# Performance work log

Hardware: AMD Instinct MI355X
Metric: run time of the kernel (lower is better)

The kernel has to match this reference:

```python
import jax, jax.numpy as jnp
import numpy as np

N = 100000      # num POIs (nodes)
M = 20000       # num trajectories (hyperedges)
NNZ = 1000000   # incidence entries
D = 128         # emb_dim
NUM_LAYERS = 3
NEG_SLOPE = 0.2  # PyG HypergraphConv leaky_relu default


def setup_inputs() -> dict:
    key = jax.random.key(0)
    ks = jax.random.split(key, 8)
    pois_embs = jax.random.normal(ks[0], (N, D), jnp.float32)
    traj_embs = jax.random.normal(ks[1], (M, D), jnp.float32)
    hyperedge_weight = jax.random.uniform(ks[2], (M,), jnp.float32)
    node_idx = jax.random.randint(ks[3], (NNZ,), 0, N, jnp.int32)
    edge_idx = jax.random.randint(ks[4], (NNZ,), 0, M, jnp.int32)
    # learned params of the shared HypergraphConv layer (heads=1, concat)
    W_lin = jax.random.normal(ks[5], (D, D), jnp.float32) / np.sqrt(D).astype(np.float32)
    att = jax.random.normal(ks[6], (2 * D,), jnp.float32) * 0.1
    bias = jnp.zeros((D,), jnp.float32)
    return dict(pois_embs=pois_embs, traj_embs=traj_embs,
                hyperedge_weight=hyperedge_weight,
                node_idx=node_idx, edge_idx=edge_idx,
                W_lin=W_lin, att=att, bias=bias)


def _segment_softmax(scores, seg, num_seg):
    smax = jax.ops.segment_max(scores, seg, num_segments=num_seg)
    smax = jnp.where(jnp.isfinite(smax), smax, 0.0)  # guard empty segments
    ex = jnp.exp(scores - smax[seg])
    den = jax.ops.segment_sum(ex, seg, num_segments=num_seg)
    return ex / (den[seg] + 1e-16)


def _hconv(x, traj_embs, hyperedge_weight, node_idx, edge_idx, W_lin, att, bias):
    # x: [N, D] node feats; traj_embs: [M, D] hyperedge feats
    xt = x @ W_lin            # [N, D]  lin(x)
    et = traj_embs @ W_lin    # [M, D]  lin(hyperedge_attr)
    # attention logits per incidence pair (additive decomposition of cat*att)
    s_n = xt @ att[:D]        # [N]
    s_e = et @ att[D:]        # [M]
    alpha = jax.nn.leaky_relu(s_n[node_idx] + s_e[edge_idx], NEG_SLOPE)  # [NNZ]
    alpha = _segment_softmax(alpha, node_idx, N)  # softmax grouped by node
    # degree normalizations: D = sum_e H_ve * w_e, B = |e|
    Ddeg = jax.ops.segment_sum(hyperedge_weight[edge_idx], node_idx, num_segments=N)
    Dinv = jnp.where(Ddeg > 0, 1.0 / Ddeg, 0.0)
    Bdeg = jax.ops.segment_sum(jnp.ones((NNZ,), xt.dtype), edge_idx, num_segments=M)
    Binv = jnp.where(Bdeg > 0, 1.0 / Bdeg, 0.0)
    # node -> edge: B^{-1} H^T (alpha * x)
    msg1 = (alpha * Binv[edge_idx])[:, None] * xt[node_idx]        # [NNZ, D]
    edge_out = jax.ops.segment_sum(msg1, edge_idx, num_segments=M)  # [M, D]
    # edge -> node: D^{-1} H (alpha * edge_out)
    msg2 = (alpha * Dinv[node_idx])[:, None] * edge_out[edge_idx]   # [NNZ, D]
    out = jax.ops.segment_sum(msg2, node_idx, num_segments=N)       # [N, D]
    return out + bias


def reference(pois_embs, traj_embs, hyperedge_weight, node_idx, edge_idx, W_lin, att, bias):
    cur = pois_embs
    acc = pois_embs  # running sum of stacked layer outputs (incl. input)
    for _ in range(NUM_LAYERS):
        cur = _hconv(cur, traj_embs, hyperedge_weight, node_idx, edge_idx, W_lin, att, bias) + cur
        acc = acc + cur
    return acc / jnp.asarray(NUM_LAYERS + 1, acc.dtype)  # mean over stack
```

## Files before the change

kernel.cpp:

```cpp
#include <hip/hip_runtime.h>
#include <cstdint>
#include <cstddef>

#define DIM 128
#define NEG_SLOPE 0.2f

typedef __attribute__((ext_vector_type(8))) short short8v;
typedef __attribute__((ext_vector_type(4))) float float4v;

__device__ __forceinline__ float bf_lo(uint u) { return __uint_as_float(u << 16); }
__device__ __forceinline__ float bf_hi(uint u) { return __uint_as_float(u & 0xffff0000u); }
__device__ __forceinline__ uint f2bf(float f) {
  uint u = __float_as_uint(f);
  return (u + 0x7fffu + ((u >> 16) & 1u)) >> 16;
}
__device__ __forceinline__ uint pack_bf2(float lo, float hi) {
  return f2bf(lo) | (f2bf(hi) << 16);
}
__device__ __forceinline__ float lrelu(float x) {
  return x >= 0.0f ? x : NEG_SLOPE * x;
}

__global__ void wswz_kernel(const float* __restrict__ W, ushort* __restrict__ Wswz)
{
  int i = blockIdx.x * 256 + threadIdx.x;
  int j = i & 7, lane = (i >> 3) & 63, nt = (i >> 9) & 7, kt = i >> 12;
  int k = kt * 32 + (lane >> 4) * 8 + j;
  int col = nt * 16 + (lane & 15);
  Wswz[i] = (ushort)f2bf(W[k * 128 + col]);
}

__global__ void poisbf_kernel(const float* __restrict__ pois,
                              uint4* __restrict__ pois_bf, int N_, int NP)
{
  int i = blockIdx.x * 256 + threadIdx.x;
  if (i >= NP * 16) return;
  int row = i >> 4;
  uint4 o;
  if (row < N_) {
    const float* src = pois + (size_t)i * 8;
    float4 f0 = *(const float4*)src;
    float4 f1 = *(const float4*)(src + 4);
    o.x = pack_bf2(f0.x, f0.y); o.y = pack_bf2(f0.z, f0.w);
    o.z = pack_bf2(f1.x, f1.y); o.w = pack_bf2(f1.z, f1.w);
  } else { o.x = o.y = o.z = o.w = 0; }
  pois_bf[i] = o;
}

__global__ __launch_bounds__(256) void gemm_mfma_kernel(
    const ushort* __restrict__ Xb, const ushort* __restrict__ Wswz,
    const float* __restrict__ att, ushort* __restrict__ Yb,
    float* __restrict__ s_n, int rowsN)
{
  __shared__ ushort st[64 * 128];
  int tid = threadIdx.x;
  int w = tid >> 6, lane = tid & 63;
  int q = lane >> 4, c = lane & 15;
  int r0b = blockIdx.x * 64;
  int r0 = r0b + w * 16;
  float4v acc[8];
#pragma unroll
  for (int nt = 0; nt < 8; ++nt) acc[nt] = (float4v){0.f, 0.f, 0.f, 0.f};
  const ushort* arow = Xb + (size_t)(r0 + c) * DIM + q * 8;
#pragma unroll
  for (int kt = 0; kt < 4; ++kt) {
    short8v a = *(const short8v*)(arow + kt * 32);
#pragma unroll
    for (int nt = 0; nt < 8; ++nt) {
      short8v b = *(const short8v*)(Wswz + ((((kt << 3) + nt) << 9) + (lane << 3)));
      acc[nt] = __builtin_amdgcn_mfma_f32_16x16x32_bf16(a, b, acc[nt], 0, 0, 0);
    }
  }
  float av[8];
#pragma unroll
  for (int nt = 0; nt < 8; ++nt) av[nt] = att[nt * 16 + c];
  float p0 = 0, p1 = 0, p2 = 0, p3 = 0;
#pragma unroll
  for (int nt = 0; nt < 8; ++nt) {
    p0 = fmaf(acc[nt][0], av[nt], p0);
    p1 = fmaf(acc[nt][1], av[nt], p1);
    p2 = fmaf(acc[nt][2], av[nt], p2);
    p3 = fmaf(acc[nt][3], av[nt], p3);
  }
#pragma unroll
  for (int m = 8; m >= 1; m >>= 1) {
    p0 += __shfl_xor(p0, m, 64);
    p1 += __shfl_xor(p1, m, 64);
    p2 += __shfl_xor(p2, m, 64);
    p3 += __shfl_xor(p3, m, 64);
  }
  if (c == 0) {
    int rb = r0 + q * 4;
    if (rb + 0 < rowsN) s_n[rb + 0] = p0;
    if (rb + 1 < rowsN) s_n[rb + 1] = p1;
    if (rb + 2 < rowsN) s_n[rb + 2] = p2;
    if (rb + 3 < rowsN) s_n[rb + 3] = p3;
  }
  ushort* sw = st + w * 2048;
#pragma unroll
  for (int nt = 0; nt < 8; ++nt) {
    sw[(q * 4 + 0) * 128 + nt * 16 + c] = (ushort)f2bf(acc[nt][0]);
    sw[(q * 4 + 1) * 128 + nt * 16 + c] = (ushort)f2bf(acc[nt][1]);
    sw[(q * 4 + 2) * 128 + nt * 16 + c] = (ushort)f2bf(acc[nt][2]);
    sw[(q * 4 + 3) * 128 + nt * 16 + c] = (ushort)f2bf(acc[nt][3]);
  }
  __syncthreads();
#pragma unroll
  for (int it = 0; it < 4; ++it) {
    int idx = tid + it * 256;
    int row = idx >> 4, seg = idx & 15;
    *(uint4*)(Yb + (size_t)(r0b + row) * DIM + seg * 8) =
        *(const uint4*)&st[row * 128 + seg * 8];
  }
}

__global__ __launch_bounds__(256) void se_kernel(
    const float* __restrict__ traj, const float* __restrict__ W,
    const float* __restrict__ att, const float* __restrict__ hw,
    float* __restrict__ s_e, float2* __restrict__ se_hw, int M_)
{
  __shared__ float wv[128];
  int tid = threadIdx.x;
  if (tid < 128) {
    const float* wr = W + (size_t)tid * 128;
    float acc = 0.0f;
#pragma unroll 4
    for (int k = 0; k < 128; ++k) acc = fmaf(wr[k], att[DIM + k], acc);
    wv[tid] = acc;
  }
  __syncthreads();
  int e = blockIdx.x * 4 + (tid >> 6);
  int lane = tid & 63;
  if (e >= M_) return;
  const float* row = traj + (size_t)e * DIM;
  float v = row[lane] * wv[lane] + row[lane + 64] * wv[lane + 64];
#pragma unroll
  for (int d = 32; d > 0; d >>= 1) v += __shfl_down(v, d, 64);
  if (lane == 0) {
    s_e[e] = v;
    float2 g; g.x = v; g.y = hw[e];
    se_hw[e] = g;
  }
}

__global__ void hist_rank_kernel(const int* __restrict__ node_idx,
                                 const int* __restrict__ edge_idx,
                                 int* __restrict__ ncnt, int* __restrict__ ecnt,
                                 int* __restrict__ r_n, int* __restrict__ r_e,
                                 int nnz)
{
  int j = (blockIdx.x * blockDim.x + threadIdx.x) * 2;
  if (j >= nnz) return;
  if (j + 2 <= nnz) {
    int2 e = *(const int2*)&edge_idx[j];
    int2 n = *(const int2*)&node_idx[j];
    int a0 = atomicAdd(&ecnt[e.x], 1);
    int a1 = atomicAdd(&ecnt[e.y], 1);
    int b0 = atomicAdd(&ncnt[n.x], 1);
    int b1 = atomicAdd(&ncnt[n.y], 1);
    *(int2*)&r_e[j] = make_int2(a0, a1);
    *(int2*)&r_n[j] = make_int2(b0, b1);
  } else {
    r_e[j] = atomicAdd(&ecnt[edge_idx[j]], 1);
    r_n[j] = atomicAdd(&ncnt[node_idx[j]], 1);
  }
}

__global__ __launch_bounds__(1024) void scan_block_kernel(
    const int* __restrict__ cnt, int* __restrict__ off,
    int* __restrict__ partials, int nbins)
{
  __shared__ int ws[16];
  int tid = threadIdx.x, lane = tid & 63, wid = tid >> 6;
  int base = blockIdx.x * 4096 + tid * 4;
  int x0 = base + 0 < nbins ? cnt[base + 0] : 0;
  int x1 = base + 1 < nbins ? cnt[base + 1] : 0;
  int x2 = base + 2 < nbins ? cnt[base + 2] : 0;
  int x3 = base + 3 < nbins ? cnt[base + 3] : 0;
  int t = x0 + x1 + x2 + x3;
  int v = t;
#pragma unroll
  for (int d = 1; d < 64; d <<= 1) {
    int y = __shfl_up(v, d, 64);
    if (lane >= d) v += y;
  }
  if (lane == 63) ws[wid] = v;
  __syncthreads();
  if (tid < 16) {
    int s = ws[tid];
#pragma unroll
    for (int d = 1; d < 16; d <<= 1) {
      int y = __shfl_up(s, d, 16);
      if (tid >= d) s += y;
    }
    ws[tid] = s;
  }
  __syncthreads();
  int pre = (wid > 0 ? ws[wid - 1] : 0) + (v - t);
  if (base + 0 < nbins) off[base + 0] = pre;
  if (base + 1 < nbins) off[base + 1] = pre + x0;
  if (base + 2 < nbins) off[base + 2] = pre + x0 + x1;
  if (base + 3 < nbins) off[base + 3] = pre + x0 + x1 + x2;
  if (tid == 0) partials[blockIdx.x] = ws[15];
}

__global__ __launch_bounds__(64) void scan_partials_kernel(
    int* __restrict__ partials, int nb)
{
  int lane = threadIdx.x;
  int t = lane < nb ? partials[lane] : 0;
  int v = t;
#pragma unroll
  for (int d = 1; d < 64; d <<= 1) {
    int y = __shfl_up(v, d, 64);
    if (lane >= d) v += y;
  }
  if (lane < nb) partials[lane] = v - t;
  if (lane == 63) partials[nb] = v;
}

__global__ void add_off_kernel(int* __restrict__ off,
                               const int* __restrict__ partials,
                               int nbins, int nb)
{
  int i = blockIdx.x * blockDim.x + threadIdx.x;
  if (i < nbins) off[i] += partials[i >> 12];
  if (i == 0) off[nbins] = partials[nb];
}

__global__ void scatter_edge_kernel(const int* __restrict__ node_idx,
                                    const int* __restrict__ edge_idx,
                                    const int* __restrict__ r_e,
                                    const int* __restrict__ eoff,
                                    int* __restrict__ nd_e, int nnz)
{
  int j = (blockIdx.x * blockDim.x + threadIdx.x) * 4;
  if (j >= nnz) return;
  if (j + 4 <= nnz) {
    int4 e = *(const int4*)&edge_idx[j];
    int4 n = *(const int4*)&node_idx[j];
    int4 re = *(const int4*)&r_e[j];
    nd_e[eoff[e.x] + re.x] = n.x;
    nd_e[eoff[e.y] + re.y] = n.y;
    nd_e[eoff[e.z] + re.z] = n.z;
    nd_e[eoff[e.w] + re.w] = n.w;
  } else {
    for (int k = j; k < nnz; ++k) nd_e[eoff[edge_idx[k]] + r_e[k]] = node_idx[k];
  }
}

__global__ void scatter_node_kernel(const int* __restrict__ node_idx,
                                    const int* __restrict__ edge_idx,
                                    const int* __restrict__ r_n,
                                    const int* __restrict__ noff,
                                    int* __restrict__ eidx_n, int nnz)
{
  int j = (blockIdx.x * blockDim.x + threadIdx.x) * 4;
  if (j >= nnz) return;
  if (j + 4 <= nnz) {
    int4 e = *(const int4*)&edge_idx[j];
    int4 n = *(const int4*)&node_idx[j];
    int4 rn = *(const int4*)&r_n[j];
    eidx_n[noff[n.x] + rn.x] = e.x;
    eidx_n[noff[n.y] + rn.y] = e.y;
    eidx_n[noff[n.z] + rn.z] = e.z;
    eidx_n[noff[n.w] + rn.w] = e.w;
  } else {
    for (int k = j; k < nnz; ++k) eidx_n[noff[node_idx[k]] + r_n[k]] = edge_idx[k];
  }
}

__global__ void softstat_kernel(const int* __restrict__ noff,
                                const int* __restrict__ eidx_n,
                                const float* __restrict__ s_n,
                                const float2* __restrict__ se_hw,
                                float2* __restrict__ ns2,
                                float* __restrict__ Dinv, int N_)
{
  int n = blockIdx.x * blockDim.x + threadIdx.x;
  if (n >= N_) return;
  int s = noff[n], e1 = noff[n + 1];
  float sn = s_n[n];
  float m = -INFINITY, den = 0.0f, d = 0.0f;
  int t = s;
  for (; t + 4 <= e1; t += 4) {
    int i0 = eidx_n[t], i1 = eidx_n[t + 1], i2 = eidx_n[t + 2], i3 = eidx_n[t + 3];
    float2 g0 = se_hw[i0], g1 = se_hw[i1], g2 = se_hw[i2], g3 = se_hw[i3];
    float l0 = lrelu(sn + g0.x), l1 = lrelu(sn + g1.x);
    float l2 = lrelu(sn + g2.x), l3 = lrelu(sn + g3.x);
    float mm = fmaxf(fmaxf(fmaxf(l0, l1), fmaxf(l2, l3)), m);
    den = den * __expf(m - mm) + __expf(l0 - mm) + __expf(l1 - mm)
        + __expf(l2 - mm) + __expf(l3 - mm);
    m = mm;
    d += g0.y + g1.y + g2.y + g3.y;
  }
  for (; t < e1; ++t) {
    float2 g = se_hw[eidx_n[t]];
    float l = lrelu(sn + g.x);
    float mm = fmaxf(l, m);
    den = den * __expf(m - mm) + __expf(l - mm);
    m = mm;
    d += g.y;
  }
  if (s == e1) m = 0.0f;
  float2 r;
  r.x = sn;
  r.y = m + __logf(den + 1e-16f);
  ns2[n] = r;
  Dinv[n] = d > 0.0f ? 1.0f / d : 0.0f;
}

__global__ __launch_bounds__(256) void msg1_kernel(
    const int* __restrict__ eoff, const int* __restrict__ nd_e,
    const float2* __restrict__ ns2, const float* __restrict__ s_e,
    const ushort* __restrict__ xt, uint* __restrict__ eo, int M_)
{
  int e = blockIdx.x * (blockDim.x >> 6) + (threadIdx.x >> 6);
  int lane = threadIdx.x & 63;
  if (e >= M_) return;
  int s = eoff[e], t1 = eoff[e + 1];
  int len = t1 - s;
  float binv = len > 0 ? 1.0f / (float)len : 0.0f;
  float se = s_e[e];
  const uint* xt4 = (const uint*)xt + lane;
  float2 acc = {0.0f, 0.0f};
  int t = s;
  for (; t + 8 <= t1; t += 8) {
    int n0 = nd_e[t],     n1 = nd_e[t + 1], n2 = nd_e[t + 2], n3 = nd_e[t + 3];
    int n4 = nd_e[t + 4], n5 = nd_e[t + 5], n6 = nd_e[t + 6], n7 = nd_e[t + 7];
    float2 q0 = ns2[n0], q1 = ns2[n1], q2 = ns2[n2], q3 = ns2[n3];
    float2 q4 = ns2[n4], q5 = ns2[n5], q6 = ns2[n6], q7 = ns2[n7];
    uint u0 = xt4[(size_t)n0 * 64], u1 = xt4[(size_t)n1 * 64];
    uint u2 = xt4[(size_t)n2 * 64], u3 = xt4[(size_t)n3 * 64];
    uint u4 = xt4[(size_t)n4 * 64], u5 = xt4[(size_t)n5 * 64];
    uint u6 = xt4[(size_t)n6 * 64], u7 = xt4[(size_t)n7 * 64];
    float c0 = __expf(lrelu(q0.x + se) - q0.y);
    float c1 = __expf(lrelu(q1.x + se) - q1.y);
    float c2 = __expf(lrelu(q2.x + se) - q2.y);
    float c3 = __expf(lrelu(q3.x + se) - q3.y);
    float c4 = __expf(lrelu(q4.x + se) - q4.y);
    float c5 = __expf(lrelu(q5.x + se) - q5.y);
    float c6 = __expf(lrelu(q6.x + se) - q6.y);
    float c7 = __expf(lrelu(q7.x + se) - q7.y);
    acc.x = fmaf(c0, bf_lo(u0), acc.x); acc.y = fmaf(c0, bf_hi(u0), acc.y);
    acc.x = fmaf(c1, bf_lo(u1), acc.x); acc.y = fmaf(c1, bf_hi(u1), acc.y);
    acc.x = fmaf(c2, bf_lo(u2), acc.x); acc.y = fmaf(c2, bf_hi(u2), acc.y);
    acc.x = fmaf(c3, bf_lo(u3), acc.x); acc.y = fmaf(c3, bf_hi(u3), acc.y);
    acc.x = fmaf(c4, bf_lo(u4), acc.x); acc.y = fmaf(c4, bf_hi(u4), acc.y);
    acc.x = fmaf(c5, bf_lo(u5), acc.x); acc.y = fmaf(c5, bf_hi(u5), acc.y);
    acc.x = fmaf(c6, bf_lo(u6), acc.x); acc.y = fmaf(c6, bf_hi(u6), acc.y);
    acc.x = fmaf(c7, bf_lo(u7), acc.x); acc.y = fmaf(c7, bf_hi(u7), acc.y);
  }
  for (; t < t1; ++t) {
    int nd = nd_e[t];
    float2 q = ns2[nd];
    uint u = xt4[(size_t)nd * 64];
    float c = __expf(lrelu(q.x + se) - q.y);
    acc.x = fmaf(c, bf_lo(u), acc.x);
    acc.y = fmaf(c, bf_hi(u), acc.y);
  }
  eo[(size_t)e * (DIM / 2) + lane] = pack_bf2(acc.x * binv, acc.y * binv);
}

__global__ __launch_bounds__(256) void msg2_kernel(
    const int* __restrict__ noff, const int* __restrict__ eidx_n,
    const float2* __restrict__ ns2, const float* __restrict__ Dinv,
    const float* __restrict__ s_e, const uint* __restrict__ eo,
    const float* __restrict__ bias,
    const float* __restrict__ cur_in, const float* __restrict__ acc_in,
    float* __restrict__ cur_out, uint* __restrict__ curbf_out,
    float* __restrict__ acc_out, int last, int N_)
{
  int n = blockIdx.x * (blockDim.x >> 6) + (threadIdx.x >> 6);
  int lane = threadIdx.x & 63;
  if (n >= N_) return;
  int s = noff[n], t1 = noff[n + 1];
  float2 nsv = ns2[n];
  float sn = nsv.x, lz = nsv.y;
  const uint* eo4 = eo + lane;
  float2 acc = {0.0f, 0.0f};
  int t = s;
  for (; t + 8 <= t1; t += 8) {
    int e0 = eidx_n[t],     e1 = eidx_n[t + 1], e2 = eidx_n[t + 2], e3 = eidx_n[t + 3];
    int e4 = eidx_n[t + 4], e5 = eidx_n[t + 5], e6 = eidx_n[t + 6], e7 = eidx_n[t + 7];
    float x0 = s_e[e0], x1 = s_e[e1], x2 = s_e[e2], x3 = s_e[e3];
    float x4 = s_e[e4], x5 = s_e[e5], x6 = s_e[e6], x7 = s_e[e7];
    uint u0 = eo4[(size_t)e0 * 64], u1 = eo4[(size_t)e1 * 64];
    uint u2 = eo4[(size_t)e2 * 64], u3 = eo4[(size_t)e3 * 64];
    uint u4 = eo4[(size_t)e4 * 64], u5 = eo4[(size_t)e5 * 64];
    uint u6 = eo4[(size_t)e6 * 64], u7 = eo4[(size_t)e7 * 64];
    float c0 = __expf(lrelu(sn + x0) - lz);
    float c1 = __expf(lrelu(sn + x1) - lz);
    float c2 = __expf(lrelu(sn + x2) - lz);
    float c3 = __expf(lrelu(sn + x3) - lz);
    float c4 = __expf(lrelu(sn + x4) - lz);
    float c5 = __expf(lrelu(sn + x5) - lz);
    float c6 = __expf(lrelu(sn + x6) - lz);
    float c7 = __expf(lrelu(sn + x7) - lz);
    acc.x = fmaf(c0, bf_lo(u0), acc.x); acc.y = fmaf(c0, bf_hi(u0), acc.y);
    acc.x = fmaf(c1, bf_lo(u1), acc.x); acc.y = fmaf(c1, bf_hi(u1), acc.y);
    acc.x = fmaf(c2, bf_lo(u2), acc.x); acc.y = fmaf(c2, bf_hi(u2), acc.y);
    acc.x = fmaf(c3, bf_lo(u3), acc.x); acc.y = fmaf(c3, bf_hi(u3), acc.y);
    acc.x = fmaf(c4, bf_lo(u4), acc.x); acc.y = fmaf(c4, bf_hi(u4), acc.y);
    acc.x = fmaf(c5, bf_lo(u5), acc.x); acc.y = fmaf(c5, bf_hi(u5), acc.y);
    acc.x = fmaf(c6, bf_lo(u6), acc.x); acc.y = fmaf(c6, bf_hi(u6), acc.y);
    acc.x = fmaf(c7, bf_lo(u7), acc.x); acc.y = fmaf(c7, bf_hi(u7), acc.y);
  }
  for (; t < t1; ++t) {
    int e = eidx_n[t];
    uint u = eo4[(size_t)e * 64];
    float c = __expf(lrelu(sn + s_e[e]) - lz);
    acc.x = fmaf(c, bf_lo(u), acc.x);
    acc.y = fmaf(c, bf_hi(u), acc.y);
  }
  float sc = Dinv[n];
  float2 b = ((const float2*)bias)[lane];
  size_t idx = (size_t)n * DIM + lane * 2;
  float cx = cur_in[idx]     + acc.x * sc + b.x;
  float cy = cur_in[idx + 1] + acc.y * sc + b.y;
  if (last) {
    acc_out[idx]     = (acc_in[idx]     + cx) * 0.25f;
    acc_out[idx + 1] = (acc_in[idx + 1] + cy) * 0.25f;
  } else {
    cur_out[idx] = cx; cur_out[idx + 1] = cy;
    curbf_out[(size_t)n * 64 + lane] = pack_bf2(cx, cy);
    acc_out[idx]     = acc_in[idx]     + cx;
    acc_out[idx + 1] = acc_in[idx + 1] + cy;
  }
}

static inline int cdiv(int a, int b) { return (a + b - 1) / b; }

extern "C" void kernel_launch(void* const* d_in, const int* in_sizes, int n_in,
                              void* d_out, int out_size, void* d_ws, size_t ws_size,
                              hipStream_t stream)
{
  const float* pois = (const float*)d_in[0];
  const float* traj = (const float*)d_in[1];
  const float* hw   = (const float*)d_in[2];
  const int* node_idx = (const int*)d_in[3];
  const int* edge_idx = (const int*)d_in[4];
  const float* W    = (const float*)d_in[5];
  const float* att  = (const float*)d_in[6];
  const float* bias = (const float*)d_in[7];
  float* dout = (float*)d_out;

  const int N   = in_sizes[0] / DIM;
  const int M   = in_sizes[2];
  const int NNZ = in_sizes[3];
  const int NP  = (N + 63) & ~63;

  char* p = (char*)d_ws;
  auto alloc = [&](size_t bytes) -> void* {
    void* r = (void*)p;
    p += (bytes + 255) & ~(size_t)255;
    return r;
  };
  ushort* xt_bf   = (ushort*)alloc((size_t)NP * DIM * 2);
  ushort* cur_bf  = (ushort*)alloc((size_t)NP * DIM * 2);
  ushort* pois_bf = (ushort*)alloc((size_t)NP * DIM * 2);
  ushort* W_swz   = (ushort*)alloc(16384 * 2);
  uint*   eo_bf = (uint*)alloc((size_t)M * (DIM / 2) * 4);
  float*  cur   = (float*)alloc((size_t)N * DIM * 4);
  float2* ns2   = (float2*)alloc((size_t)N * 8);
  float*  s_e  = (float*)alloc((size_t)M * 4);
  float2* se_hw = (float2*)alloc((size_t)M * 8);
  float*  s_n  = (float*)alloc((size_t)N * 4);
  float*  Dinv = (float*)alloc((size_t)N * 4);
  int* ecnt = (int*)alloc((size_t)M * 4);
  int* ncnt = (int*)alloc((size_t)N * 4);
  int* eoff = (int*)alloc((size_t)(M + 1) * 4);
  int* noff = (int*)alloc((size_t)(N + 1) * 4);
  int* r_e  = (int*)alloc((size_t)NNZ * 4);
  int* r_n  = (int*)alloc((size_t)NNZ * 4);
  int* nd_e   = (int*)alloc((size_t)NNZ * 4);
  int* eidx_n = (int*)alloc((size_t)NNZ * 4);
  int* part_e = (int*)alloc(65 * 4);
  int* part_n = (int*)alloc(65 * 4);
  (void)ws_size;

  const int nbE = cdiv(M, 4096), nbN = cdiv(N, 4096);

  hipMemsetAsync(ecnt, 0, (size_t)M * 4, stream);
  hipMemsetAsync(ncnt, 0, (size_t)N * 4, stream);
  hist_rank_kernel<<<cdiv(NNZ, 512), 256, 0, stream>>>(node_idx, edge_idx, ncnt, ecnt, r_n, r_e, NNZ);
  scan_block_kernel<<<nbE, 1024, 0, stream>>>(ecnt, eoff, part_e, M);
  scan_block_kernel<<<nbN, 1024, 0, stream>>>(ncnt, noff, part_n, N);
  scan_partials_kernel<<<1, 64, 0, stream>>>(part_e, nbE);
  scan_partials_kernel<<<1, 64, 0, stream>>>(part_n, nbN);
  add_off_kernel<<<cdiv(M, 256), 256, 0, stream>>>(eoff, part_e, M, nbE);
  add_off_kernel<<<cdiv(N, 256), 256, 0, stream>>>(noff, part_n, N, nbN);
  scatter_edge_kernel<<<cdiv(NNZ, 1024), 256, 0, stream>>>(node_idx, edge_idx, r_e, eoff, nd_e, NNZ);
  scatter_node_kernel<<<cdiv(NNZ, 1024), 256, 0, stream>>>(node_idx, edge_idx, r_n, noff, eidx_n, NNZ);

  wswz_kernel<<<64, 256, 0, stream>>>(W, W_swz);
  se_kernel<<<cdiv(M, 4), 256, 0, stream>>>(traj, W, att, hw, s_e, se_hw, M);
  poisbf_kernel<<<cdiv(NP * 16, 256), 256, 0, stream>>>(pois, (uint4*)pois_bf, N, NP);

  for (int layer = 0; layer < 3; ++layer) {
    const ushort* gin = (layer == 0) ? pois_bf : cur_bf;
    gemm_mfma_kernel<<<NP / 64, 256, 0, stream>>>(gin, W_swz, att, xt_bf, s_n, N);
    softstat_kernel<<<cdiv(N, 256), 256, 0, stream>>>(noff, eidx_n, s_n, se_hw, ns2, Dinv, N);
    msg1_kernel<<<cdiv(M, 4), 256, 0, stream>>>(eoff, nd_e, ns2, s_e, xt_bf, eo_bf, M);
    const float* cin = (layer == 0) ? pois : cur;
    const float* ain = (layer == 0) ? pois : dout;
    int last = (layer == 2) ? 1 : 0;
    msg2_kernel<<<cdiv(N, 4), 256, 0, stream>>>(noff, eidx_n, ns2, Dinv, s_e, eo_bf,
                                                bias, cin, ain, cur, (uint*)cur_bf,
                                                dout, last, N);
  }
}
```

Baseline: 753.7 us.

## Fuse next-layer softmax statistics into msg2 and drop running accumulator writes

Computes s_n as a row dot with W@att[:D] (wv1) instead of inside the GEMM epilogue. The online softmax max/denominator for the next layer is computed at the end of msg2, which removes the per-layer softstat launch after layer 0. The running-sum output is no longer read and written every layer; the last layer instead reconstructs the mean from pois, cur1 and cur2. This trades extra gather passes over s_e in msg2 and an extra N×D buffer for fewer kernels and less full-size accumulator traffic. s_n now comes from fp32 cur rather than the bf16 GEMM result, which changes rounding slightly.

```diff
diff --git a/kernel.cpp b/kernel.cpp
--- a/kernel.cpp
+++ b/kernel.cpp
@@ -31,26 +31,34 @@
 }
 
 __global__ void poisbf_kernel(const float* __restrict__ pois,
-                              uint4* __restrict__ pois_bf, int N_, int NP)
+                              const float* __restrict__ wv1,
+                              uint4* __restrict__ pois_bf,
+                              float* __restrict__ s_n0, int N_, int NP)
 {
   int i = blockIdx.x * 256 + threadIdx.x;
   if (i >= NP * 16) return;
-  int row = i >> 4;
+  int row = i >> 4, seg = i & 15;
   uint4 o;
+  float p = 0.0f;
   if (row < N_) {
     const float* src = pois + (size_t)i * 8;
     float4 f0 = *(const float4*)src;
     float4 f1 = *(const float4*)(src + 4);
     o.x = pack_bf2(f0.x, f0.y); o.y = pack_bf2(f0.z, f0.w);
     o.z = pack_bf2(f1.x, f1.y); o.w = pack_bf2(f1.z, f1.w);
+    const float* wseg = wv1 + seg * 8;
+    p = f0.x*wseg[0] + f0.y*wseg[1] + f0.z*wseg[2] + f0.w*wseg[3]
+      + f1.x*wseg[4] + f1.y*wseg[5] + f1.z*wseg[6] + f1.w*wseg[7];
   } else { o.x = o.y = o.z = o.w = 0; }
   pois_bf[i] = o;
+#pragma unroll
+  for (int m = 8; m >= 1; m >>= 1) p += __shfl_xor(p, m, 64);
+  if (seg == 0 && row < N_) s_n0[row] = p;
 }
 
 __global__ __launch_bounds__(256) void gemm_mfma_kernel(
     const ushort* __restrict__ Xb, const ushort* __restrict__ Wswz,
-    const float* __restrict__ att, ushort* __restrict__ Yb,
-    float* __restrict__ s_n, int rowsN)
+    ushort* __restrict__ Yb)
 {
   __shared__ ushort st[64 * 128];
   int tid = threadIdx.x;
@@ -71,31 +79,6 @@
       acc[nt] = __builtin_amdgcn_mfma_f32_16x16x32_bf16(a, b, acc[nt], 0, 0, 0);
     }
   }
-  float av[8];
-#pragma unroll
-  for (int nt = 0; nt < 8; ++nt) av[nt] = att[nt * 16 + c];
-  float p0 = 0, p1 = 0, p2 = 0, p3 = 0;
-#pragma unroll
-  for (int nt = 0; nt < 8; ++nt) {
-    p0 = fmaf(acc[nt][0], av[nt], p0);
-    p1 = fmaf(acc[nt][1], av[nt], p1);
-    p2 = fmaf(acc[nt][2], av[nt], p2);
-    p3 = fmaf(acc[nt][3], av[nt], p3);
-  }
-#pragma unroll
-  for (int m = 8; m >= 1; m >>= 1) {
-    p0 += __shfl_xor(p0, m, 64);
-    p1 += __shfl_xor(p1, m, 64);
-    p2 += __shfl_xor(p2, m, 64);
-    p3 += __shfl_xor(p3, m, 64);
-  }
-  if (c == 0) {
-    int rb = r0 + q * 4;
-    if (rb + 0 < rowsN) s_n[rb + 0] = p0;
-    if (rb + 1 < rowsN) s_n[rb + 1] = p1;
-    if (rb + 2 < rowsN) s_n[rb + 2] = p2;
-    if (rb + 3 < rowsN) s_n[rb + 3] = p3;
-  }
   ushort* sw = st + w * 2048;
 #pragma unroll
   for (int nt = 0; nt < 8; ++nt) {
@@ -112,6 +95,20 @@
     *(uint4*)(Yb + (size_t)(r0b + row) * DIM + seg * 8) =
         *(const uint4*)&st[row * 128 + seg * 8];
   }
+}
+
+__global__ __launch_bounds__(256) void rowdot_kernel(
+    const float* __restrict__ X, const float* __restrict__ a,
+    float* __restrict__ out, int rows)
+{
+  int w = blockIdx.x * (blockDim.x >> 6) + (threadIdx.x >> 6);
+  int lane = threadIdx.x & 63;
+  if (w >= rows) return;
+  const float* row = X + (size_t)w * DIM;
+  float v = row[lane] * a[lane] + row[lane + 64] * a[lane + 64];
+#pragma unroll
+  for (int d = 32; d > 0; d >>= 1) v += __shfl_down(v, d, 64);
+  if (lane == 0) out[w] = v;
 }
 
 __global__ __launch_bounds__(256) void se_kernel(
@@ -364,12 +361,13 @@
 
 __global__ __launch_bounds__(256) void msg2_kernel(
     const int* __restrict__ noff, const int* __restrict__ eidx_n,
-    const float2* __restrict__ ns2, const float* __restrict__ Dinv,
+    float2* __restrict__ ns2, const float* __restrict__ Dinv,
     const float* __restrict__ s_e, const uint* __restrict__ eo,
-    const float* __restrict__ bias,
-    const float* __restrict__ cur_in, const float* __restrict__ acc_in,
+    const float* __restrict__ bias, const float* __restrict__ wv1,
+    const float* __restrict__ cur_in,
     float* __restrict__ cur_out, uint* __restrict__ curbf_out,
-    float* __restrict__ acc_out, int last, int N_)
+    const float* __restrict__ pois, const float* __restrict__ cur1,
+    float* __restrict__ dout, int last, int N_)
 {
   int n = blockIdx.x * (blockDim.x >> 6) + (threadIdx.x >> 6);
   int lane = threadIdx.x & 63;
@@ -416,16 +414,32 @@
   float sc = Dinv[n];
   float2 b = ((const float2*)bias)[lane];
   size_t idx = (size_t)n * DIM + lane * 2;
-  float cx = cur_in[idx]     + acc.x * sc + b.x;
-  float cy = cur_in[idx + 1] + acc.y * sc + b.y;
+  float dx = acc.x * sc + b.x;
+  float dy = acc.y * sc + b.y;
+  float cix = cur_in[idx], ciy = cur_in[idx + 1];
   if (last) {
-    acc_out[idx]     = (acc_in[idx]     + cx) * 0.25f;
-    acc_out[idx + 1] = (acc_in[idx + 1] + cy) * 0.25f;
-  } else {
-    cur_out[idx] = cx; cur_out[idx + 1] = cy;
-    curbf_out[(size_t)n * 64 + lane] = pack_bf2(cx, cy);
-    acc_out[idx]     = acc_in[idx]     + cx;
-    acc_out[idx + 1] = acc_in[idx + 1] + cy;
+    dout[idx]     = 0.25f * (pois[idx]     + cur1[idx]     + 2.0f * cix + dx);
+    dout[idx + 1] = 0.25f * (pois[idx + 1] + cur1[idx + 1] + 2.0f * ciy + dy);
+    return;
+  }
+  float cx = cix + dx, cy = ciy + dy;
+  cur_out[idx] = cx; cur_out[idx + 1] = cy;
+  curbf_out[(size_t)n * 64 + lane] = pack_bf2(cx, cy);
+  float2 wv = ((const float2*)wv1)[lane];
+  float pv = cx * wv.x + cy * wv.y;
+#pragma unroll
+  for (int m = 32; m >= 1; m >>= 1) pv += __shfl_xor(pv, m, 64);
+  float m2 = -INFINITY, den = 0.0f;
+  for (int t2 = s; t2 < t1; ++t2) {
+    float l = lrelu(pv + s_e[eidx_n[t2]]);
+    float mm = fmaxf(l, m2);
+    den = den * __expf(m2 - mm) + __expf(l - mm);
+    m2 = mm;
+  }
+  if (s == t1) m2 = 0.0f;
+  if (lane == 0) {
+    float2 r; r.x = pv; r.y = m2 + __logf(den + 1e-16f);
+    ns2[n] = r;
   }
 }
 
@@ -461,12 +475,14 @@
   ushort* pois_bf = (ushort*)alloc((size_t)NP * DIM * 2);
   ushort* W_swz   = (ushort*)alloc(16384 * 2);
   uint*   eo_bf = (uint*)alloc((size_t)M * (DIM / 2) * 4);
-  float*  cur   = (float*)alloc((size_t)N * DIM * 4);
+  float*  cur1  = (float*)alloc((size_t)N * DIM * 4);
+  float*  cur2  = (float*)alloc((size_t)N * DIM * 4);
   float2* ns2   = (float2*)alloc((size_t)N * 8);
   float*  s_e  = (float*)alloc((size_t)M * 4);
   float2* se_hw = (float2*)alloc((size_t)M * 8);
-  float*  s_n  = (float*)alloc((size_t)N * 4);
+  float*  s_n0 = (float*)alloc((size_t)N * 4);
   float*  Dinv = (float*)alloc((size_t)N * 4);
+  float*  wv1  = (float*)alloc(DIM * 4);
   int* ecnt = (int*)alloc((size_t)M * 4);
   int* ncnt = (int*)alloc((size_t)N * 4);
   int* eoff = (int*)alloc((size_t)(M + 1) * 4);
@@ -495,18 +511,19 @@
 
   wswz_kernel<<<64, 256, 0, stream>>>(W, W_swz);
   se_kernel<<<cdiv(M, 4), 256, 0, stream>>>(traj, W, att, hw, s_e, se_hw, M);
-  poisbf_kernel<<<cdiv(NP * 16, 256), 256, 0, stream>>>(pois, (uint4*)pois_bf, N, NP);
+  rowdot_kernel<<<cdiv(DIM, 4), 256, 0, stream>>>(W, att, wv1, DIM);
+  poisbf_kernel<<<cdiv(NP * 16, 256), 256, 0, stream>>>(pois, wv1, (uint4*)pois_bf, s_n0, N, NP);
+  softstat_kernel<<<cdiv(N, 256), 256, 0, stream>>>(noff, eidx_n, s_n0, se_hw, ns2, Dinv, N);
 
   for (int layer = 0; layer < 3; ++layer) {
     const ushort* gin = (layer == 0) ? pois_bf : cur_bf;
-    gemm_mfma_kernel<<<NP / 64, 256, 0, stream>>>(gin, W_swz, att, xt_bf, s_n, N);
-    softstat_kernel<<<cdiv(N, 256), 256, 0, stream>>>(noff, eidx_n, s_n, se_hw, ns2, Dinv, N);
+    gemm_mfma_kernel<<<NP / 64, 256, 0, stream>>>(gin, W_swz, xt_bf);
     msg1_kernel<<<cdiv(M, 4), 256, 0, stream>>>(eoff, nd_e, ns2, s_e, xt_bf, eo_bf, M);
-    const float* cin = (layer == 0) ? pois : cur;
-    const float* ain = (layer == 0) ? pois : dout;
+    const float* cin = (layer == 0) ? pois : (layer == 1 ? cur1 : cur2);
+    float* cout = (layer == 0) ? cur1 : cur2;
     int last = (layer == 2) ? 1 : 0;
     msg2_kernel<<<cdiv(N, 4), 256, 0, stream>>>(noff, eidx_n, ns2, Dinv, s_e, eo_bf,
-                                                bias, cin, ain, cur, (uint*)cur_bf,
-                                                dout, last, N);
-  }
-}
+                                                bias, wv1, cin, cout, (uint*)cur_bf,
+                                                pois, cur1, dout, last, N);
+  }
+}
```

New measurement: 849.9 us. +12.8%, slower.
